# Kernel tuning notes

Measured on AMD Instinct MI355X. Metric: run time of the kernel, lower is better.

The kernel has to match this reference:

```python
import jax, jax.numpy as jnp
import numpy as np

N1 = 100000  # source cloud size (x1)
N2 = 100000  # target cloud size (x2)
F = 64       # point feature dim
E = 1600000  # number of radius edges (avg 16 neighbors)
H = 128      # MLP hidden/out dim


def setup_inputs() -> dict:
    key = jax.random.key(0)
    ks = jax.random.split(key, 12)
    s = 0.05
    return {
        "x1_features": jax.random.normal(ks[0], (N1, F), jnp.float32),
        "x1_pos": jax.random.normal(ks[1], (N1, 3), jnp.float32),
        "x2_features": jax.random.normal(ks[2], (N2, F), jnp.float32),
        "x2_pos": jax.random.normal(ks[3], (N2, 3), jnp.float32),
        "W1": jax.random.normal(ks[4], (2 * F + 3, H), jnp.float32) * s,
        "b1": jnp.zeros((H,), jnp.float32),
        "W2": jax.random.normal(ks[5], (H, H), jnp.float32) * s,
        "b2": jnp.zeros((H,), jnp.float32),
        "W3": jax.random.normal(ks[6], (H, H), jnp.float32) * s,
        "b3": jnp.zeros((H,), jnp.float32),
        "edge_src": jax.random.randint(ks[7], (E,), 0, N1, jnp.int32),
        "edge_dst": jax.random.randint(ks[8], (E,), 0, N2, jnp.int32),
    }


def reference(x1_features, x1_pos, x2_features, x2_pos,
              W1, b1, W2, b2, W3, b3, edge_src, edge_dst):
    # message(x_i, x_j, pos_i, pos_j): i = target (x2, edge_dst), j = source (x1, edge_src)
    # msg = cat([x_i, x_j, pos_j - pos_i], dim=1)  -> [E, 2F+3]
    msg = jnp.concatenate(
        [x2_features[edge_dst],
         x1_features[edge_src],
         x1_pos[edge_src] - x2_pos[edge_dst]], axis=1)
    # MLP (Linear+ReLU x3, FastFlow3D make_mlp style)
    h = jax.nn.relu(msg @ W1 + b1)
    h = jax.nn.relu(h @ W2 + b2)
    h = jax.nn.relu(h @ W3 + b3)
    # scatter-max aggregation onto x2 nodes; PyG fills empty segments with 0
    out = jax.ops.segment_max(h, edge_dst, num_segments=N2)
    out = jnp.where(jnp.isneginf(out), 0.0, out)
    return out, x2_pos
```

## Files before the change

### kernel.cpp

```cpp
#include <hip/hip_runtime.h>
#include <hip/hip_bf16.h>

#define DEV __device__ __forceinline__

typedef short bf16x8 __attribute__((ext_vector_type(8)));
typedef float f32x16 __attribute__((ext_vector_type(16)));
typedef unsigned short u16x2 __attribute__((ext_vector_type(2)));

static constexpr int FDIM = 64;
static constexpr int HH   = 128;
static constexpr int TM   = 128;
static constexpr int CH   = 4096;
static constexpr int NCH  = 27;
static constexpr int WT_ELEMS = NCH * 2048;

DEV unsigned pack2(float a, float b) {
    union { __hip_bfloat162 h; unsigned u; } cv;
    cv.h.x = __float2bfloat16(a);
    cv.h.y = __float2bfloat16(b);
    return cv.u;
}
DEV unsigned short f2bf(float f) {
    union { __hip_bfloat16 h; unsigned short u; } cv;
    cv.h = __float2bfloat16(f);
    return cv.u;
}
DEV unsigned pmax2(unsigned a, unsigned b) {
    u16x2 av = __builtin_bit_cast(u16x2, a);
    u16x2 bv = __builtin_bit_cast(u16x2, b);
    return __builtin_bit_cast(unsigned, __builtin_elementwise_max(av, bv));
}
template <int CTRL>
DEV int dppmov(int x) {
    return __builtin_amdgcn_update_dpp(x, x, CTRL, 0xf, 0xf, false);
}

__global__ void k_cvt(const float* __restrict__ src, unsigned short* __restrict__ dst, int n8) {
    int i = blockIdx.x * 256 + threadIdx.x;
    if (i < n8) {
        float4 a = *(const float4*)(src + (size_t)i * 8);
        float4 b = *(const float4*)(src + (size_t)i * 8 + 4);
        uint4 o;
        o.x = pack2(a.x, a.y); o.y = pack2(a.z, a.w);
        o.z = pack2(b.x, b.y); o.w = pack2(b.z, b.w);
        *(uint4*)(dst + (size_t)i * 8) = o;
    }
}

__global__ void k_wprep(const float* __restrict__ W1, const float* __restrict__ b1,
                        const float* __restrict__ W2, const float* __restrict__ b2,
                        const float* __restrict__ W3, const float* __restrict__ b3,
                        unsigned short* __restrict__ wt) {
    int i = blockIdx.x * 256 + threadIdx.x;
    if (i >= WT_ELEMS) return;
    int c = i >> 11, r = i & 2047;
    int n = r >> 4, half = (r >> 3) & 1, e = r & 7;
    int layer = c / 9, ks = c % 9;
    int k = ks * 16 + half * 8 + e;
    float v = 0.f;
    if (layer == 0) {
        if (k < 131) v = W1[k * HH + n];
        else if (k == 131) v = b1[n];
    } else {
        const float* W = (layer == 1) ? W2 : W3;
        const float* b = (layer == 1) ? b2 : b3;
        if (k < 128) v = W[k * HH + n];
        else if (k == 128) v = b[n];
    }
    wt[i] = f2bf(v);
}

__global__ void k_hist(const int* __restrict__ edst, int* __restrict__ cnt, int E) {
    int e = blockIdx.x * 256 + threadIdx.x;
    if (e < E) atomicAdd(&cnt[edst[e]], 1);
}

__global__ void k_scan_part(const int* __restrict__ cnt, int* __restrict__ partial, int n2) {
    __shared__ int sm[256];
    int t = threadIdx.x;
    int base = blockIdx.x * 1024 + t * 4;
    int s = 0;
#pragma unroll
    for (int j = 0; j < 4; j++) { int idx = base + j; if (idx < n2) s += cnt[idx]; }
    sm[t] = s; __syncthreads();
    for (int off = 128; off > 0; off >>= 1) {
        if (t < off) sm[t] += sm[t + off];
        __syncthreads();
    }
    if (t == 0) partial[blockIdx.x] = sm[0];
}

__global__ void k_scan_top(int* __restrict__ partial, int nb) {
    __shared__ int sm[256];
    int t = threadIdx.x;
    int v = (t < nb) ? partial[t] : 0;
    sm[t] = v; __syncthreads();
    for (int off = 1; off < 256; off <<= 1) {
        int add = (t >= off) ? sm[t - off] : 0;
        __syncthreads();
        sm[t] += add;
        __syncthreads();
    }
    if (t < nb) partial[t] = sm[t] - v;
}

__global__ void k_scan_down(const int* __restrict__ cnt, const int* __restrict__ partial,
                            int* __restrict__ cursor, int n2) {
    __shared__ int sm[256];
    int t = threadIdx.x;
    int base = blockIdx.x * 1024 + t * 4;
    int c[4]; int s = 0;
#pragma unroll
    for (int j = 0; j < 4; j++) { int idx = base + j; c[j] = (idx < n2) ? cnt[idx] : 0; s += c[j]; }
    sm[t] = s; __syncthreads();
    for (int off = 1; off < 256; off <<= 1) {
        int add = (t >= off) ? sm[t - off] : 0;
        __syncthreads();
        sm[t] += add;
        __syncthreads();
    }
    int run = partial[blockIdx.x] + (sm[t] - s);
#pragma unroll
    for (int j = 0; j < 4; j++) {
        int idx = base + j;
        if (idx < n2) cursor[idx] = run;
        run += c[j];
    }
}

__global__ void k_fill(const int* __restrict__ edst, const int* __restrict__ esrc,
                       int* __restrict__ cursor, int2* __restrict__ csr_sd, int E) {
    int e = blockIdx.x * 256 + threadIdx.x;
    if (e < E) {
        int d = edst[e];
        int p = atomicAdd(&cursor[d], 1);
        csr_sd[p] = make_int2(esrc[e], d);
    }
}

DEV f32x16 zerov() {
    f32x16 v;
#pragma unroll
    for (int i = 0; i < 16; i++) v[i] = 0.f;
    return v;
}
DEV float relu(float x) { return fmaxf(x, 0.f); }

DEV void layer_reg(const char* __restrict__ wl, const unsigned pkin[32],
                   unsigned pkout[32], int l31, int hh, unsigned biasw) {
    unsigned xv[16];
#pragma unroll
    for (int ks = 0; ks < 8; ks++) {
        unsigned t0 = hh ? pkin[4 * ks + 0] : pkin[4 * ks + 2];
        unsigned t1 = hh ? pkin[4 * ks + 1] : pkin[4 * ks + 3];
        xv[2 * ks + 0] = (unsigned)__shfl_xor((int)t0, 32, 64);
        xv[2 * ks + 1] = (unsigned)__shfl_xor((int)t1, 32, 64);
    }
#pragma unroll
    for (int rt = 0; rt < 4; rt++) {
        const char* arow = wl + (rt * 32 + l31) * 32 + hh * 16;
        f32x16 acc = zerov();
#pragma unroll
        for (int ks = 0; ks < 8; ks++) {
            union { unsigned u[4]; bf16x8 v; } B;
            B.u[0] = hh ? xv[2 * ks + 0]   : pkin[4 * ks + 0];
            B.u[1] = hh ? xv[2 * ks + 1]   : pkin[4 * ks + 1];
            B.u[2] = hh ? pkin[4 * ks + 2] : xv[2 * ks + 0];
            B.u[3] = hh ? pkin[4 * ks + 3] : xv[2 * ks + 1];
            bf16x8 A = *(const bf16x8*)(arow + ks * CH);
            acc = __builtin_amdgcn_mfma_f32_32x32x16_bf16(A, B.v, acc, 0, 0, 0);
        }
        {
            union { unsigned u[4]; bf16x8 v; } B;
            B.u[0] = biasw; B.u[1] = 0u; B.u[2] = 0u; B.u[3] = 0u;
            bf16x8 A = *(const bf16x8*)(arow + 8 * CH);
            acc = __builtin_amdgcn_mfma_f32_32x32x16_bf16(A, B.v, acc, 0, 0, 0);
        }
#pragma unroll
        for (int g = 0; g < 4; g++) {
            pkout[8 * rt + 2 * g + 0] = pack2(relu(acc[4 * g + 0]), relu(acc[4 * g + 1]));
            pkout[8 * rt + 2 * g + 1] = pack2(relu(acc[4 * g + 2]), relu(acc[4 * g + 3]));
        }
    }
}

template <bool SORTED, bool BF16SRC>
__global__ __launch_bounds__(256, 6) void k_main(
    const float* __restrict__ x1f, const float* __restrict__ x1p,
    const float* __restrict__ x2f, const float* __restrict__ x2p,
    const char* __restrict__ xb1, const char* __restrict__ xb2,
    const char* __restrict__ wt,
    const int2* __restrict__ csr_sd,
    const int* __restrict__ edge_src, const int* __restrict__ edge_dst,
    float* __restrict__ out, int E) {
    const int tid  = threadIdx.x;
    const int lane = tid & 63;
    const int wv   = tid >> 6;
    const int l31  = lane & 31;
    const int hh   = lane >> 5;
    const int r    = wv * 32 + l31;
    const int slot = blockIdx.x * TM + r;
    const bool ok  = slot < E;

    int d = -1, s = 0;
    if (ok) {
        if (SORTED) { int2 sd = csr_sd[slot]; s = sd.x; d = sd.y; }
        else        { d = edge_dst[slot]; s = edge_src[slot]; }
    }
    const int dg = (d < 0) ? 0 : d;
    const int sg = s;

    bf16x8 Bv[9];
    if (BF16SRC) {
        const char* bx2 = xb2 + (size_t)dg * (2 * FDIM);
        const char* bx1 = xb1 + (size_t)sg * (2 * FDIM);
#pragma unroll
        for (int ks = 0; ks < 4; ks++)
            Bv[ks] = *(const bf16x8*)(bx2 + (2 * ks + hh) * 16);
#pragma unroll
        for (int ks = 4; ks < 8; ks++)
            Bv[ks] = *(const bf16x8*)(bx1 + (2 * (ks - 4) + hh) * 16);
    } else {
        const float* fx2 = x2f + (size_t)dg * FDIM;
        const float* fx1 = x1f + (size_t)sg * FDIM;
#pragma unroll
        for (int ks = 0; ks < 8; ks++) {
            const float* b = (ks < 4) ? (fx2 + (2 * ks + hh) * 8)
                                      : (fx1 + (2 * (ks - 4) + hh) * 8);
            float4 a0 = *(const float4*)(b);
            float4 a1 = *(const float4*)(b + 4);
            union { unsigned u[4]; bf16x8 v; } B;
            B.u[0] = pack2(a0.x, a0.y); B.u[1] = pack2(a0.z, a0.w);
            B.u[2] = pack2(a1.x, a1.y); B.u[3] = pack2(a1.z, a1.w);
            Bv[ks] = B.v;
        }
    }
    {
        float dx = 0.f, dy = 0.f, dz = 0.f;
        if (ok) {
            dx = x1p[sg * 3 + 0] - x2p[dg * 3 + 0];
            dy = x1p[sg * 3 + 1] - x2p[dg * 3 + 1];
            dz = x1p[sg * 3 + 2] - x2p[dg * 3 + 2];
        }
        union { unsigned u[4]; bf16x8 v; } P;
        P.u[0] = hh ? 0u : pack2(dx, dy);
        P.u[1] = hh ? 0u : pack2(dz, 1.0f);
        P.u[2] = 0u; P.u[3] = 0u;
        Bv[8] = P.v;
    }

    unsigned pkA[32], pkB[32];
#pragma unroll
    for (int rt = 0; rt < 4; rt++) {
        const char* arow = wt + (rt * 32 + l31) * 32 + hh * 16;
        f32x16 acc = zerov();
#pragma unroll
        for (int ks = 0; ks < 9; ks++) {
            bf16x8 A = *(const bf16x8*)(arow + ks * CH);
            acc = __builtin_amdgcn_mfma_f32_32x32x16_bf16(A, Bv[ks], acc, 0, 0, 0);
        }
#pragma unroll
        for (int g = 0; g < 4; g++) {
            pkA[8 * rt + 2 * g + 0] = pack2(relu(acc[4 * g + 0]), relu(acc[4 * g + 1]));
            pkA[8 * rt + 2 * g + 1] = pack2(relu(acc[4 * g + 2]), relu(acc[4 * g + 3]));
        }
    }

    const unsigned biasw = hh ? 0u : 0x00003F80u;
    layer_reg(wt + 9 * CH,  pkA, pkB, l31, hh, biasw);
    layer_reg(wt + 18 * CH, pkB, pkA, l31, hh, biasw);

#define SCAN_STEP(CTRL, EXTRA)                                            \
    {                                                                     \
        int dsft = dppmov<CTRL>(d);                                       \
        bool take = (dsft == d) EXTRA;                                    \
        _Pragma("unroll")                                                 \
        for (int u = 0; u < 32; u++) {                                    \
            int sv = dppmov<CTRL>((int)pkA[u]);                           \
            unsigned mx = pmax2(pkA[u], (unsigned)sv);                    \
            pkA[u] = take ? mx : pkA[u];                                  \
        }                                                                 \
    }
    SCAN_STEP(0x111, )
    SCAN_STEP(0x112, )
    SCAN_STEP(0x114, )
    SCAN_STEP(0x118, )
    SCAN_STEP(0x142, && (l31 >= 16))
#undef SCAN_STEP

    const int dn = __shfl_down(d, 1, 32);
    const int dp = __shfl_up(d, 1, 32);
    unsigned long long startm = __ballot(dp != d) | 0x0000000100000001ull;
    const bool isflush = (d >= 0) && ((l31 == 31) || (dn != d));
    if (isflush) {
        unsigned long long below = startm & (~0ull >> (63 - lane));
        int sbit = 63 - __builtin_clzll(below);
        bool interior = ((sbit & 31) != 0) && (l31 != 31);
        float* orow = out + (size_t)d * HH;
        if (interior) {
#pragma unroll
            for (int g = 0; g < 16; g++) {
                const int F = 32 * (g >> 2) + 8 * (g & 3) + 4 * hh;
                unsigned w0 = pkA[2 * g], w1 = pkA[2 * g + 1];
                float4 v;
                v.x = __uint_as_float(w0 << 16);
                v.y = __uint_as_float(w0 & 0xffff0000u);
                v.z = __uint_as_float(w1 << 16);
                v.w = __uint_as_float(w1 & 0xffff0000u);
                *(float4*)(orow + F) = v;
            }
        } else {
            int* op = (int*)orow;
#pragma unroll
            for (int u = 0; u < 32; u++) {
                const int feat = 32 * (u >> 3) + 8 * ((u >> 1) & 3) + 4 * hh + 2 * (u & 1);
                unsigned w = pkA[u];
                float lo = __uint_as_float(w << 16);
                float hi = __uint_as_float(w & 0xffff0000u);
                if (lo > 0.f) atomicMax(op + feat,     __float_as_int(lo));
                if (hi > 0.f) atomicMax(op + feat + 1, __float_as_int(hi));
            }
        }
    }
}

extern "C" void kernel_launch(void* const* d_in, const int* in_sizes, int n_in,
                              void* d_out, int out_size, void* d_ws, size_t ws_size,
                              hipStream_t stream) {
    const float* x1f = (const float*)d_in[0];
    const float* x1p = (const float*)d_in[1];
    const float* x2f = (const float*)d_in[2];
    const float* x2p = (const float*)d_in[3];
    const float* W1  = (const float*)d_in[4];
    const float* b1  = (const float*)d_in[5];
    const float* W2  = (const float*)d_in[6];
    const float* b2  = (const float*)d_in[7];
    const float* W3  = (const float*)d_in[8];
    const float* b3  = (const float*)d_in[9];
    const int* esrc  = (const int*)d_in[10];
    const int* edst  = (const int*)d_in[11];
    const int E  = in_sizes[10];
    const int N1 = in_sizes[1] / 3;
    const int N2 = in_sizes[3] / 3;
    float* out = (float*)d_out;

    size_t off = 0;
    auto take = [&](size_t bytes) { size_t o = off; off = (off + bytes + 255) & ~(size_t)255; return o; };
    size_t o_cnt = take(4 * (size_t)N2);
    size_t o_cur = take(4 * (size_t)N2);
    size_t o_par = take(4 * 256);
    size_t o_csd = take(8 * (size_t)E);
    size_t o_wt  = take(2 * (size_t)WT_ELEMS);
    size_t need_csr = off;
    size_t o_x1  = take(2 * (size_t)N1 * FDIM);
    size_t o_x2  = take(2 * (size_t)N2 * FDIM);
    size_t need_bf = off;

    const int NB = (N2 + 1023) / 1024;
    bool use_csr = (need_csr <= ws_size) && (NB <= 256);
    bool use_bf  = (need_bf <= ws_size);

    char* ws = (char*)d_ws;
    unsigned short* wt = use_csr ? (unsigned short*)(ws + o_wt) : (unsigned short*)ws;
    int*  cnt    = (int*)(ws + o_cnt);
    int*  cursor = (int*)(ws + o_cur);
    int*  part   = (int*)(ws + o_par);
    int2* csr_sd = (int2*)(ws + o_csd);
    char* xb1    = ws + o_x1;
    char* xb2    = ws + o_x2;

    (void)hipMemsetAsync(out, 0, (size_t)N2 * HH * 4, stream);
    (void)hipMemcpyAsync(out + (size_t)N2 * HH, x2p, (size_t)N2 * 3 * 4,
                         hipMemcpyDeviceToDevice, stream);

    k_wprep<<<(WT_ELEMS + 255) / 256, 256, 0, stream>>>(W1, b1, W2, b2, W3, b3, wt);

    if (use_bf) {
        int n8_1 = N1 * FDIM / 8, n8_2 = N2 * FDIM / 8;
        k_cvt<<<(n8_1 + 255) / 256, 256, 0, stream>>>(x1f, (unsigned short*)xb1, n8_1);
        k_cvt<<<(n8_2 + 255) / 256, 256, 0, stream>>>(x2f, (unsigned short*)xb2, n8_2);
    }

    const int grid = (E + TM - 1) / TM;
    if (use_csr) {
        (void)hipMemsetAsync(cnt, 0, 4 * (size_t)N2, stream);
        k_hist<<<(E + 255) / 256, 256, 0, stream>>>(edst, cnt, E);
        k_scan_part<<<NB, 256, 0, stream>>>(cnt, part, N2);
        k_scan_top<<<1, 256, 0, stream>>>(part, NB);
        k_scan_down<<<NB, 256, 0, stream>>>(cnt, part, cursor, N2);
        k_fill<<<(E + 255) / 256, 256, 0, stream>>>(edst, esrc, cursor, csr_sd, E);
        if (use_bf)
            k_main<true, true><<<grid, 256, 0, stream>>>(
                x1f, x1p, x2f, x2p, xb1, xb2, (const char*)wt, csr_sd, esrc, edst, out, E);
        else
            k_main<true, false><<<grid, 256, 0, stream>>>(
                x1f, x1p, x2f, x2p, xb1, xb2, (const char*)wt, csr_sd, esrc, edst, out, E);
    } else {
        if (use_bf)
            k_main<false, true><<<grid, 256, 0, stream>>>(
                x1f, x1p, x2f, x2p, xb1, xb2, (const char*)wt, csr_sd, esrc, edst, out, E);
        else
            k_main<false, false><<<grid, 256, 0, stream>>>(
                x1f, x1p, x2f, x2p, xb1, xb2, (const char*)wt, csr_sd, esrc, edst, out, E);
    }
}
```

Measured before the change: 693.8 us.

## Merge boundary segment partials across wavefronts in shared memory before atomics

Doubles the block to 8 wavefronts (256 edges per block) and changes launch bounds to 512 threads. The first and last segment runs of each half-wave are no longer flushed with global atomicMax. They are written to a shared-memory partial table, and one wavefront combines adjacent rows with the same destination. Only a block's first segment and its final run use atomics; runs fully inside the block get plain stores. This cuts global atomic traffic at segment boundaries, at the cost of a block-wide barrier and a serial merge done by a single wavefront.

After: 1.293 ms. +86.4%, slower.

```diff
diff --git a/kernel.cpp b/kernel.cpp
--- a/kernel.cpp
+++ b/kernel.cpp
@@ -9,10 +9,14 @@
 
 static constexpr int FDIM = 64;
 static constexpr int HH   = 128;
-static constexpr int TM   = 128;
+static constexpr int NW   = 8;
+static constexpr int TM   = NW * 32;
 static constexpr int CH   = 4096;
 static constexpr int NCH  = 27;
 static constexpr int WT_ELEMS = NCH * 2048;
+
+static constexpr int PROW = 68;
+static constexpr int NROW = 2 * NW;
 
 DEV unsigned pack2(float a, float b) {
     union { __hip_bfloat162 h; unsigned u; } cv;
@@ -185,7 +189,7 @@
 }
 
 template <bool SORTED, bool BF16SRC>
-__global__ __launch_bounds__(256, 6) void k_main(
+__global__ __launch_bounds__(512, 8) void k_main(
     const float* __restrict__ x1f, const float* __restrict__ x1p,
     const float* __restrict__ x2f, const float* __restrict__ x2p,
     const char* __restrict__ xb1, const char* __restrict__ xb2,
@@ -193,6 +197,9 @@
     const int2* __restrict__ csr_sd,
     const int* __restrict__ edge_src, const int* __restrict__ edge_dst,
     float* __restrict__ out, int E) {
+    __shared__ unsigned part[NROW][PROW];
+    __shared__ int pdst[NROW];
+
     const int tid  = threadIdx.x;
     const int lane = tid & 63;
     const int wv   = tid >> 6;
@@ -201,6 +208,8 @@
     const int r    = wv * 32 + l31;
     const int slot = blockIdx.x * TM + r;
     const bool ok  = slot < E;
+
+    if (lane == 0) { pdst[2 * wv] = -1; pdst[2 * wv + 1] = -1; }
 
     int d = -1, s = 0;
     if (ok) {
@@ -295,9 +304,10 @@
     if (isflush) {
         unsigned long long below = startm & (~0ull >> (63 - lane));
         int sbit = 63 - __builtin_clzll(below);
-        bool interior = ((sbit & 31) != 0) && (l31 != 31);
-        float* orow = out + (size_t)d * HH;
-        if (interior) {
+        bool firstrun = ((sbit & 31) == 0);
+        bool lastrun  = (l31 == 31);
+        if (!firstrun && !lastrun) {
+            float* orow = out + (size_t)d * HH;
 #pragma unroll
             for (int g = 0; g < 16; g++) {
                 const int F = 32 * (g >> 2) + 8 * (g & 3) + 4 * hh;
@@ -310,16 +320,57 @@
                 *(float4*)(orow + F) = v;
             }
         } else {
-            int* op = (int*)orow;
-#pragma unroll
-            for (int u = 0; u < 32; u++) {
-                const int feat = 32 * (u >> 3) + 8 * ((u >> 1) & 3) + 4 * hh + 2 * (u & 1);
-                unsigned w = pkA[u];
-                float lo = __uint_as_float(w << 16);
-                float hi = __uint_as_float(w & 0xffff0000u);
-                if (lo > 0.f) atomicMax(op + feat,     __float_as_int(lo));
-                if (hi > 0.f) atomicMax(op + feat + 1, __float_as_int(hi));
+            if (firstrun) {
+                const int row = 2 * wv;
+                pdst[row] = d;
+#pragma unroll
+                for (int g = 0; g < 16; g++)
+                    *(uint2*)&part[row][32 * hh + 2 * g] = make_uint2(pkA[2 * g], pkA[2 * g + 1]);
             }
+            if (lastrun) {
+                const int row = 2 * wv + 1;
+                pdst[row] = d;
+#pragma unroll
+                for (int g = 0; g < 16; g++)
+                    *(uint2*)&part[row][32 * hh + 2 * g] = make_uint2(pkA[2 * g], pkA[2 * g + 1]);
+            }
+        }
+    }
+    __syncthreads();
+
+    if (wv == 0) {
+        const int p  = lane;
+        const int u  = lane & 31;
+        const int ph = lane >> 5;
+        const int feat = 32 * (u >> 3) + 8 * ((u >> 1) & 3) + 4 * ph + 2 * (u & 1);
+        int cur = -1, rs = 0;
+        unsigned m = 0;
+#pragma unroll
+        for (int rr = 0; rr < NROW; rr++) {
+            int dd = pdst[rr];
+            if (dd != cur) {
+                if (cur >= 0) {
+                    float lo = __uint_as_float(m << 16);
+                    float hi = __uint_as_float(m & 0xffff0000u);
+                    if (rs == 0) {
+                        int* op = (int*)out + (size_t)cur * HH + feat;
+                        if (lo > 0.f) atomicMax(op,     __float_as_int(lo));
+                        if (hi > 0.f) atomicMax(op + 1, __float_as_int(hi));
+                    } else {
+                        float2 v; v.x = lo; v.y = hi;
+                        *(float2*)(out + (size_t)cur * HH + feat) = v;
+                    }
+                }
+                cur = dd; rs = rr; m = 0;
+            }
+            if (dd >= 0) m = pmax2(m, part[rr][p]);
+        }
+        if (cur >= 0) {
+            float lo = __uint_as_float(m << 16);
+            float hi = __uint_as_float(m & 0xffff0000u);
+            int* op = (int*)out + (size_t)cur * HH + feat;
+            if (lo > 0.f) atomicMax(op,     __float_as_int(lo));
+            if (hi > 0.f) atomicMax(op + 1, __float_as_int(hi));
         }
     }
 }
@@ -390,17 +441,17 @@
         k_scan_down<<<NB, 256, 0, stream>>>(cnt, part, cursor, N2);
         k_fill<<<(E + 255) / 256, 256, 0, stream>>>(edst, esrc, cursor, csr_sd, E);
         if (use_bf)
-            k_main<true, true><<<grid, 256, 0, stream>>>(
+            k_main<true, true><<<grid, 512, 0, stream>>>(
                 x1f, x1p, x2f, x2p, xb1, xb2, (const char*)wt, csr_sd, esrc, edst, out, E);
         else
-            k_main<true, false><<<grid, 256, 0, stream>>>(
+            k_main<true, false><<<grid, 512, 0, stream>>>(
                 x1f, x1p, x2f, x2p, xb1, xb2, (const char*)wt, csr_sd, esrc, edst, out, E);
     } else {
         if (use_bf)
-            k_main<false, true><<<grid, 256, 0, stream>>>(
+            k_main<false, true><<<grid, 512, 0, stream>>>(
                 x1f, x1p, x2f, x2p, xb1, xb2, (const char*)wt, csr_sd, esrc, edst, out, E);
         else
-            k_main<false, false><<<grid, 256, 0, stream>>>(
+            k_main<false, false><<<grid, 512, 0, stream>>>(
                 x1f, x1p, x2f, x2p, xb1, xb2, (const char*)wt, csr_sd, esrc, edst, out, E);
     }
 }
```
